# Kernel optimization log

Measured on AMD Instinct MI355X. Metric: run time of the kernel, lower is better.

The kernel has to match this reference:

```python
import jax, jax.numpy as jnp
import numpy as np

EPS = 1e-8

def squash(s, axis=-1):
    norm = jnp.linalg.norm(s, axis=axis, keepdims=True)
    scale = norm / (1.0 + norm * norm)
    return scale * s / (norm + EPS)

def setup_inputs() -> dict:
    key = jax.random.key(0)
    k1, k2, k3, k4 = jax.random.split(key, 4)
    B = 65536
    x = jax.random.normal(k1, (B, 210), dtype=jnp.float32)
    # stacked weights/biases for the 7 Linear(30,8) primary capsules
    W_pc = jax.random.normal(k2, (7, 8, 30), dtype=jnp.float32) * (1.0 / np.sqrt(30.0))
    b_pc = jax.random.normal(k3, (7, 8), dtype=jnp.float32) * 0.01
    W = jax.random.normal(k4, (7, 12, 8, 16), dtype=jnp.float32)
    return {"x": x, "W_pc": W_pc, "b_pc": b_pc, "W": W, "num_iterations": 3}

def reference(x, W_pc, b_pc, W, num_iterations):
    B = x.shape[0]
    groups = x.reshape(B, 7, 30)                              # [B,7,30]
    # 7 parallel Linear(30,8) + squash -> primary capsules u
    u = squash(jnp.einsum('bng,nog->bno', groups, W_pc) + b_pc)  # [B,7,8]
    # prediction vectors u_hat (expand over the 12 output capsules)
    u_hat = jnp.einsum('bnj,nmjk->bnmk', u, W)                # [B,7,12,16]
    b = jnp.zeros((B, 7, 12), dtype=x.dtype)
    v = None
    for it in range(num_iterations):
        c = jax.nn.softmax(b, axis=2)                         # [B,7,12]
        s = jnp.einsum('bnm,bnmk->bmk', c, u_hat)             # [B,12,16]
        v = squash(s)
        if it < num_iterations - 1:
            b = b + jnp.einsum('bnmk,bmk->bnm', u_hat, v)
    return jnp.linalg.norm(v, axis=-1)                        # [B,12]
```

## Files before the change

### kernel.cpp

```cpp
#include <hip/hip_runtime.h>
#include <math.h>

#define GPB 8
#define THREADS 256

template<int CTRL>
__device__ __forceinline__ float dpp_add(float x) {
    int xi = __builtin_bit_cast(int, x);
    int yi = __builtin_amdgcn_update_dpp(0, xi, CTRL, 0xF, 0xF, false);
    return x + __builtin_bit_cast(float, yi);
}
__device__ __forceinline__ float row16_sum(float x) {
    x = dpp_add<0x121>(x);
    x = dpp_add<0x122>(x);
    x = dpp_add<0x124>(x);
    x = dpp_add<0x128>(x);
    return x;
}
__device__ __forceinline__ float xor16_add(float x) {
    int y = __builtin_amdgcn_ds_swizzle(__builtin_bit_cast(int, x), 0x401F);
    return x + __builtin_bit_cast(float, y);
}
__device__ __forceinline__ float rcpf_(float x) { return __builtin_amdgcn_rcpf(x); }

__global__ void transpose_W_kernel(const float* __restrict__ W,
                                   float4* __restrict__ Wt) {
    int i = blockIdx.x * blockDim.x + threadIdx.x;
    if (i < 3584) {
        int l  = i & 31;
        int r  = i >> 5;
        int q  = r & 1;
        int j  = (r >> 1) & 7;
        int n  = r >> 4;
        int kh = l >> 4;
        int t  = l & 15;
        int mm = (t < 12) ? t : 11;
        const float* src = W + (((size_t)(n * 12 + mm) * 8 + j) * 16 + kh * 8 + q * 4);
        Wt[i] = *(const float4*)src;
    }
}

__global__ __launch_bounds__(THREADS) void capsnet_kernel(
    const float* __restrict__ x,
    const float* __restrict__ W_pc,
    const float* __restrict__ b_pc,
    const float4* __restrict__ Wt,
    const int*  __restrict__ p_niter,
    float* __restrict__ out,
    int B)
{
    __shared__ float xs[GPB][210];
    __shared__ float us[GPB][56];

    const int tid = threadIdx.x;
    const int g   = tid >> 5;
    const int l   = tid & 31;
    const int kh  = l >> 4;
    const int t   = l & 15;
    int b = blockIdx.x * GPB + g;
    const bool valid_b = (b < B);
    if (!valid_b) b = B - 1;
    const int niter = *p_niter;

    {
        const float2* xrow = (const float2*)(x + (size_t)b * 210);
        float2* xdst = (float2*)&xs[g][0];
        #pragma unroll
        for (int i = 0; i < 4; ++i) {
            int idx = l + 32 * i;
            if (idx < 105) xdst[idx] = xrow[idx];
        }
    }
    __syncthreads();

    #pragma unroll
    for (int i = 0; i < 2; ++i) {
        int idx = l + 32 * i;
        if (idx < 56) {
            int n = idx >> 3;
            const float2* wrow2 = (const float2*)(W_pc + idx * 30);
            const float2* xr2   = (const float2*)&xs[g][n * 30];
            float acc = b_pc[idx];
            #pragma unroll
            for (int gg = 0; gg < 15; ++gg) {
                float2 wv = wrow2[gg];
                float2 xv = xr2[gg];
                acc += xv.x * wv.x;
                acc += xv.y * wv.y;
            }
            us[g][idx] = acc;
        }
    }
    __syncthreads();

    if (l < 7) {
        float vals[8];
        float s2 = 0.f;
        #pragma unroll
        for (int o = 0; o < 8; ++o) {
            vals[o] = us[g][l * 8 + o];
            s2 += vals[o] * vals[o];
        }
        float nrm = sqrtf(s2);
        float f = nrm * rcpf_((1.f + s2) * (nrm + 1e-8f));
        #pragma unroll
        for (int o = 0; o < 8; ++o) us[g][l * 8 + o] = vals[o] * f;
    }
    __syncthreads();

    float uh[7][8];
    #pragma unroll
    for (int n = 0; n < 7; ++n) {
        float uu[8];
        {
            float4 a  = *(const float4*)&us[g][n * 8];
            float4 c4 = *(const float4*)&us[g][n * 8 + 4];
            uu[0] = a.x;  uu[1] = a.y;  uu[2] = a.z;  uu[3] = a.w;
            uu[4] = c4.x; uu[5] = c4.y; uu[6] = c4.z; uu[7] = c4.w;
        }
        #pragma unroll
        for (int kk = 0; kk < 8; ++kk) uh[n][kk] = 0.f;
        #pragma unroll
        for (int j = 0; j < 8; ++j) {
            float uj = uu[j];
            const float4* base = Wt + (size_t)(n * 8 + j) * 64 + l;
            float4 w0 = base[0];
            float4 w1 = base[32];
            uh[n][0] += uj * w0.x;  uh[n][1] += uj * w0.y;
            uh[n][2] += uj * w0.z;  uh[n][3] += uj * w0.w;
            uh[n][4] += uj * w1.x;  uh[n][5] += uj * w1.y;
            uh[n][6] += uj * w1.z;  uh[n][7] += uj * w1.w;
        }
    }

    const bool active = (t < 12);
    float blog[7];
    float vnorm = 0.f;

    {
        float s[8];
        #pragma unroll
        for (int kk = 0; kk < 8; ++kk) s[kk] = uh[0][kk];
        #pragma unroll
        for (int n = 1; n < 7; ++n)
            #pragma unroll
            for (int kk = 0; kk < 8; ++kk) s[kk] += uh[n][kk];
        const float c0 = 1.0f / 12.0f;
        #pragma unroll
        for (int kk = 0; kk < 8; ++kk) s[kk] *= c0;
        float s2l = 0.f;
        #pragma unroll
        for (int kk = 0; kk < 8; ++kk) s2l += s[kk] * s[kk];
        float s2 = xor16_add(s2l);
        float nrm = sqrtf(s2);
        float f = nrm * rcpf_((1.f + s2) * (nrm + 1e-8f));
        if (niter == 1) {
            vnorm = f * nrm;
        } else {
            #pragma unroll
            for (int kk = 0; kk < 8; ++kk) s[kk] *= f;
            #pragma unroll
            for (int n = 0; n < 7; ++n) {
                float dl = 0.f;
                #pragma unroll
                for (int kk = 0; kk < 8; ++kk) dl += uh[n][kk] * s[kk];
                blog[n] = xor16_add(dl);
            }
        }
    }

    for (int it = 1; it < niter; ++it) {
        float c[7];
        #pragma unroll
        for (int n = 0; n < 7; ++n) {
            float e  = active ? __expf(blog[n]) : 0.f;
            float sm = row16_sum(e);
            c[n] = e * rcpf_(sm);
        }
        float s[8];
        #pragma unroll
        for (int kk = 0; kk < 8; ++kk) s[kk] = 0.f;
        #pragma unroll
        for (int n = 0; n < 7; ++n) {
            float cn = c[n];
            #pragma unroll
            for (int kk = 0; kk < 8; ++kk) s[kk] += cn * uh[n][kk];
        }
        float s2l = 0.f;
        #pragma unroll
        for (int kk = 0; kk < 8; ++kk) s2l += s[kk] * s[kk];
        float s2 = xor16_add(s2l);
        float nrm = sqrtf(s2);
        float f = nrm * rcpf_((1.f + s2) * (nrm + 1e-8f));
        if (it == niter - 1) {
            vnorm = f * nrm;
        } else {
            #pragma unroll
            for (int kk = 0; kk < 8; ++kk) s[kk] *= f;
            #pragma unroll
            for (int n = 0; n < 7; ++n) {
                float dl = 0.f;
                #pragma unroll
                for (int kk = 0; kk < 8; ++kk) dl += uh[n][kk] * s[kk];
                blog[n] += xor16_add(dl);
            }
        }
    }

    if (active && (kh == 0) && valid_b) out[(size_t)b * 12 + t] = vnorm;
}

extern "C" void kernel_launch(void* const* d_in, const int* in_sizes, int n_in,
                              void* d_out, int out_size, void* d_ws, size_t ws_size,
                              hipStream_t stream) {
    const float* x    = (const float*)d_in[0];
    const float* W_pc = (const float*)d_in[1];
    const float* b_pc = (const float*)d_in[2];
    const float* W    = (const float*)d_in[3];
    const int* niter  = (const int*)d_in[4];
    float* out = (float*)d_out;

    float4* Wt = (float4*)d_ws;

    int B = in_sizes[0] / 210;
    int blocks = (B + GPB - 1) / GPB;

    transpose_W_kernel<<<14, 256, 0, stream>>>(W, Wt);
    capsnet_kernel<<<blocks, THREADS, 0, stream>>>(x, W_pc, b_pc, Wt, niter, out, B);
}
```

Before: 224.8 us.

## Process two batch elements per 32-lane group to reuse W loads

```diff
diff --git a/kernel.cpp b/kernel.cpp
--- a/kernel.cpp
+++ b/kernel.cpp
@@ -2,6 +2,7 @@
 #include <math.h>
 
 #define GPB 8
+#define EPG 2
 #define THREADS 256
 
 template<int CTRL>
@@ -49,165 +50,189 @@
     float* __restrict__ out,
     int B)
 {
-    __shared__ float xs[GPB][210];
-    __shared__ float us[GPB][56];
+    __shared__ float xs[GPB][420];
+    __shared__ float us[GPB][EPG][56];
 
     const int tid = threadIdx.x;
     const int g   = tid >> 5;
     const int l   = tid & 31;
     const int kh  = l >> 4;
     const int t   = l & 15;
-    int b = blockIdx.x * GPB + g;
-    const bool valid_b = (b < B);
-    if (!valid_b) b = B - 1;
+    int b0 = (blockIdx.x * GPB + g) * EPG;
+    if (b0 + 1 >= B) b0 = B - 2;
     const int niter = *p_niter;
 
     {
-        const float2* xrow = (const float2*)(x + (size_t)b * 210);
+        const float2* xrow = (const float2*)(x + (size_t)b0 * 210);
         float2* xdst = (float2*)&xs[g][0];
         #pragma unroll
-        for (int i = 0; i < 4; ++i) {
+        for (int i = 0; i < 7; ++i) {
             int idx = l + 32 * i;
-            if (idx < 105) xdst[idx] = xrow[idx];
+            if (idx < 210) xdst[idx] = xrow[idx];
         }
     }
     __syncthreads();
 
     #pragma unroll
-    for (int i = 0; i < 2; ++i) {
-        int idx = l + 32 * i;
-        if (idx < 56) {
-            int n = idx >> 3;
-            const float2* wrow2 = (const float2*)(W_pc + idx * 30);
-            const float2* xr2   = (const float2*)&xs[g][n * 30];
-            float acc = b_pc[idx];
-            #pragma unroll
-            for (int gg = 0; gg < 15; ++gg) {
-                float2 wv = wrow2[gg];
-                float2 xv = xr2[gg];
-                acc += xv.x * wv.x;
-                acc += xv.y * wv.y;
-            }
-            us[g][idx] = acc;
+    for (int e = 0; e < EPG; ++e) {
+        #pragma unroll
+        for (int i = 0; i < 2; ++i) {
+            int idx = l + 32 * i;
+            if (idx < 56) {
+                int n = idx >> 3;
+                const float2* wrow2 = (const float2*)(W_pc + idx * 30);
+                const float2* xr2   = (const float2*)&xs[g][e * 210 + n * 30];
+                float acc = b_pc[idx];
+                #pragma unroll
+                for (int gg = 0; gg < 15; ++gg) {
+                    float2 wv = wrow2[gg];
+                    float2 xv = xr2[gg];
+                    acc += xv.x * wv.x;
+                    acc += xv.y * wv.y;
+                }
+                us[g][e][idx] = acc;
+            }
         }
     }
     __syncthreads();
 
-    if (l < 7) {
-        float vals[8];
-        float s2 = 0.f;
-        #pragma unroll
-        for (int o = 0; o < 8; ++o) {
-            vals[o] = us[g][l * 8 + o];
-            s2 += vals[o] * vals[o];
-        }
-        float nrm = sqrtf(s2);
-        float f = nrm * rcpf_((1.f + s2) * (nrm + 1e-8f));
-        #pragma unroll
-        for (int o = 0; o < 8; ++o) us[g][l * 8 + o] = vals[o] * f;
+    {
+        int sn = l & 15;
+        int se = l >> 4;
+        if (sn < 7) {
+            float vals[8];
+            float s2 = 0.f;
+            #pragma unroll
+            for (int o = 0; o < 8; ++o) {
+                vals[o] = us[g][se][sn * 8 + o];
+                s2 += vals[o] * vals[o];
+            }
+            float nrm = sqrtf(s2);
+            float f = nrm * rcpf_((1.f + s2) * (nrm + 1e-8f));
+            #pragma unroll
+            for (int o = 0; o < 8; ++o) us[g][se][sn * 8 + o] = vals[o] * f;
+        }
     }
     __syncthreads();
 
-    float uh[7][8];
+    float uh[EPG][7][8];
     #pragma unroll
     for (int n = 0; n < 7; ++n) {
-        float uu[8];
-        {
-            float4 a  = *(const float4*)&us[g][n * 8];
-            float4 c4 = *(const float4*)&us[g][n * 8 + 4];
-            uu[0] = a.x;  uu[1] = a.y;  uu[2] = a.z;  uu[3] = a.w;
-            uu[4] = c4.x; uu[5] = c4.y; uu[6] = c4.z; uu[7] = c4.w;
-        }
-        #pragma unroll
-        for (int kk = 0; kk < 8; ++kk) uh[n][kk] = 0.f;
+        float uu[EPG][8];
+        #pragma unroll
+        for (int e = 0; e < EPG; ++e) {
+            float4 a  = *(const float4*)&us[g][e][n * 8];
+            float4 c4 = *(const float4*)&us[g][e][n * 8 + 4];
+            uu[e][0] = a.x;  uu[e][1] = a.y;  uu[e][2] = a.z;  uu[e][3] = a.w;
+            uu[e][4] = c4.x; uu[e][5] = c4.y; uu[e][6] = c4.z; uu[e][7] = c4.w;
+        }
+        #pragma unroll
+        for (int e = 0; e < EPG; ++e)
+            #pragma unroll
+            for (int kk = 0; kk < 8; ++kk) uh[e][n][kk] = 0.f;
         #pragma unroll
         for (int j = 0; j < 8; ++j) {
-            float uj = uu[j];
             const float4* base = Wt + (size_t)(n * 8 + j) * 64 + l;
             float4 w0 = base[0];
             float4 w1 = base[32];
-            uh[n][0] += uj * w0.x;  uh[n][1] += uj * w0.y;
-            uh[n][2] += uj * w0.z;  uh[n][3] += uj * w0.w;
-            uh[n][4] += uj * w1.x;  uh[n][5] += uj * w1.y;
-            uh[n][6] += uj * w1.z;  uh[n][7] += uj * w1.w;
+            #pragma unroll
+            for (int e = 0; e < EPG; ++e) {
+                float uj = uu[e][j];
+                uh[e][n][0] += uj * w0.x;  uh[e][n][1] += uj * w0.y;
+                uh[e][n][2] += uj * w0.z;  uh[e][n][3] += uj * w0.w;
+                uh[e][n][4] += uj * w1.x;  uh[e][n][5] += uj * w1.y;
+                uh[e][n][6] += uj * w1.z;  uh[e][n][7] += uj * w1.w;
+            }
         }
     }
 
     const bool active = (t < 12);
-    float blog[7];
-    float vnorm = 0.f;
+    float blog[EPG][7];
+    float vnorm[EPG];
+    #pragma unroll
+    for (int e = 0; e < EPG; ++e) vnorm[e] = 0.f;
 
     {
-        float s[8];
-        #pragma unroll
-        for (int kk = 0; kk < 8; ++kk) s[kk] = uh[0][kk];
-        #pragma unroll
-        for (int n = 1; n < 7; ++n)
-            #pragma unroll
-            for (int kk = 0; kk < 8; ++kk) s[kk] += uh[n][kk];
-        const float c0 = 1.0f / 12.0f;
-        #pragma unroll
-        for (int kk = 0; kk < 8; ++kk) s[kk] *= c0;
-        float s2l = 0.f;
-        #pragma unroll
-        for (int kk = 0; kk < 8; ++kk) s2l += s[kk] * s[kk];
-        float s2 = xor16_add(s2l);
-        float nrm = sqrtf(s2);
-        float f = nrm * rcpf_((1.f + s2) * (nrm + 1e-8f));
-        if (niter == 1) {
-            vnorm = f * nrm;
-        } else {
-            #pragma unroll
-            for (int kk = 0; kk < 8; ++kk) s[kk] *= f;
+        #pragma unroll
+        for (int e = 0; e < EPG; ++e) {
+            float s[8];
+            #pragma unroll
+            for (int kk = 0; kk < 8; ++kk) s[kk] = uh[e][0][kk];
+            #pragma unroll
+            for (int n = 1; n < 7; ++n)
+                #pragma unroll
+                for (int kk = 0; kk < 8; ++kk) s[kk] += uh[e][n][kk];
+            const float c0 = 1.0f / 12.0f;
+            #pragma unroll
+            for (int kk = 0; kk < 8; ++kk) s[kk] *= c0;
+            float s2l = 0.f;
+            #pragma unroll
+            for (int kk = 0; kk < 8; ++kk) s2l += s[kk] * s[kk];
+            float s2 = xor16_add(s2l);
+            float nrm = sqrtf(s2);
+            float f = nrm * rcpf_((1.f + s2) * (nrm + 1e-8f));
+            if (niter == 1) {
+                vnorm[e] = f * nrm;
+            } else {
+                #pragma unroll
+                for (int kk = 0; kk < 8; ++kk) s[kk] *= f;
+                #pragma unroll
+                for (int n = 0; n < 7; ++n) {
+                    float dl = 0.f;
+                    #pragma unroll
+                    for (int kk = 0; kk < 8; ++kk) dl += uh[e][n][kk] * s[kk];
+                    blog[e][n] = xor16_add(dl);
+                }
+            }
+        }
+    }
+
+    for (int it = 1; it < niter; ++it) {
+        #pragma unroll
+        for (int e = 0; e < EPG; ++e) {
+            float c[7];
             #pragma unroll
             for (int n = 0; n < 7; ++n) {
-                float dl = 0.f;
-                #pragma unroll
-                for (int kk = 0; kk < 8; ++kk) dl += uh[n][kk] * s[kk];
-                blog[n] = xor16_add(dl);
-            }
-        }
-    }
-
-    for (int it = 1; it < niter; ++it) {
-        float c[7];
-        #pragma unroll
-        for (int n = 0; n < 7; ++n) {
-            float e  = active ? __expf(blog[n]) : 0.f;
-            float sm = row16_sum(e);
-            c[n] = e * rcpf_(sm);
-        }
-        float s[8];
-        #pragma unroll
-        for (int kk = 0; kk < 8; ++kk) s[kk] = 0.f;
-        #pragma unroll
-        for (int n = 0; n < 7; ++n) {
-            float cn = c[n];
-            #pragma unroll
-            for (int kk = 0; kk < 8; ++kk) s[kk] += cn * uh[n][kk];
-        }
-        float s2l = 0.f;
-        #pragma unroll
-        for (int kk = 0; kk < 8; ++kk) s2l += s[kk] * s[kk];
-        float s2 = xor16_add(s2l);
-        float nrm = sqrtf(s2);
-        float f = nrm * rcpf_((1.f + s2) * (nrm + 1e-8f));
-        if (it == niter - 1) {
-            vnorm = f * nrm;
-        } else {
-            #pragma unroll
-            for (int kk = 0; kk < 8; ++kk) s[kk] *= f;
+                float ev = active ? __expf(blog[e][n]) : 0.f;
+                float sm = row16_sum(ev);
+                c[n] = ev * rcpf_(sm);
+            }
+            float s[8];
+            #pragma unroll
+            for (int kk = 0; kk < 8; ++kk) s[kk] = 0.f;
             #pragma unroll
             for (int n = 0; n < 7; ++n) {
-                float dl = 0.f;
-                #pragma unroll
-                for (int kk = 0; kk < 8; ++kk) dl += uh[n][kk] * s[kk];
-                blog[n] += xor16_add(dl);
-            }
-        }
-    }
-
-    if (active && (kh == 0) && valid_b) out[(size_t)b * 12 + t] = vnorm;
+                float cn = c[n];
+                #pragma unroll
+                for (int kk = 0; kk < 8; ++kk) s[kk] += cn * uh[e][n][kk];
+            }
+            float s2l = 0.f;
+            #pragma unroll
+            for (int kk = 0; kk < 8; ++kk) s2l += s[kk] * s[kk];
+            float s2 = xor16_add(s2l);
+            float nrm = sqrtf(s2);
+            float f = nrm * rcpf_((1.f + s2) * (nrm + 1e-8f));
+            if (it == niter - 1) {
+                vnorm[e] = f * nrm;
+            } else {
+                #pragma unroll
+                for (int kk = 0; kk < 8; ++kk) s[kk] *= f;
+                #pragma unroll
+                for (int n = 0; n < 7; ++n) {
+                    float dl = 0.f;
+                    #pragma unroll
+                    for (int kk = 0; kk < 8; ++kk) dl += uh[e][n][kk] * s[kk];
+                    blog[e][n] += xor16_add(dl);
+                }
+            }
+        }
+    }
+
+    if (active && (kh == 0)) {
+        #pragma unroll
+        for (int e = 0; e < EPG; ++e)
+            out[(size_t)(b0 + e) * 12 + t] = vnorm[e];
+    }
 }
 
 extern "C" void kernel_launch(void* const* d_in, const int* in_sizes, int n_in,
@@ -223,7 +248,8 @@
     float4* Wt = (float4*)d_ws;
 
     int B = in_sizes[0] / 210;
-    int blocks = (B + GPB - 1) / GPB;
+    int elems_per_block = GPB * EPG;
+    int blocks = (B + elems_per_block - 1) / elems_per_block;
 
     transpose_W_kernel<<<14, 256, 0, stream>>>(W, Wt);
     capsnet_kernel<<<blocks, THREADS, 0, stream>>>(x, W_pc, b_pc, Wt, niter, out, B);
```

After: 474.7 us. +111.2%, slower.

## Assign one full 64-lane wavefront per batch sample instead of half-wave

Applied to the files above, without the earlier changes.

```diff
diff --git a/kernel.cpp b/kernel.cpp
--- a/kernel.cpp
+++ b/kernel.cpp
@@ -1,7 +1,7 @@
 #include <hip/hip_runtime.h>
 #include <math.h>
 
-#define GPB 8
+#define WPB 4
 #define THREADS 256
 
 template<int CTRL>
@@ -17,9 +17,11 @@
     x = dpp_add<0x128>(x);
     return x;
 }
-__device__ __forceinline__ float xor16_add(float x) {
+__device__ __forceinline__ float kq_sum(float x) {
     int y = __builtin_amdgcn_ds_swizzle(__builtin_bit_cast(int, x), 0x401F);
-    return x + __builtin_bit_cast(float, y);
+    x += __builtin_bit_cast(float, y);
+    x += __shfl_xor(x, 32, 64);
+    return x;
 }
 __device__ __forceinline__ float rcpf_(float x) { return __builtin_amdgcn_rcpf(x); }
 
@@ -27,15 +29,14 @@
                                    float4* __restrict__ Wt) {
     int i = blockIdx.x * blockDim.x + threadIdx.x;
     if (i < 3584) {
-        int l  = i & 31;
-        int r  = i >> 5;
-        int q  = r & 1;
-        int j  = (r >> 1) & 7;
-        int n  = r >> 4;
-        int kh = l >> 4;
+        int l  = i & 63;
+        int r  = i >> 6;
+        int j  = r & 7;
+        int n  = r >> 3;
+        int kq = l >> 4;
         int t  = l & 15;
         int mm = (t < 12) ? t : 11;
-        const float* src = W + (((size_t)(n * 12 + mm) * 8 + j) * 16 + kh * 8 + q * 4);
+        const float* src = W + (((size_t)(n * 12 + mm) * 8 + j) * 16 + kq * 4);
         Wt[i] = *(const float4*)src;
     }
 }
@@ -49,47 +50,43 @@
     float* __restrict__ out,
     int B)
 {
-    __shared__ float xs[GPB][210];
-    __shared__ float us[GPB][56];
+    __shared__ float xs[WPB][210];
+    __shared__ float us[WPB][56];
 
     const int tid = threadIdx.x;
-    const int g   = tid >> 5;
-    const int l   = tid & 31;
-    const int kh  = l >> 4;
+    const int w   = tid >> 6;
+    const int l   = tid & 63;
+    const int kq  = l >> 4;
     const int t   = l & 15;
-    int b = blockIdx.x * GPB + g;
+    int b = blockIdx.x * WPB + w;
     const bool valid_b = (b < B);
     if (!valid_b) b = B - 1;
     const int niter = *p_niter;
 
     {
         const float2* xrow = (const float2*)(x + (size_t)b * 210);
-        float2* xdst = (float2*)&xs[g][0];
-        #pragma unroll
-        for (int i = 0; i < 4; ++i) {
-            int idx = l + 32 * i;
+        float2* xdst = (float2*)&xs[w][0];
+        #pragma unroll
+        for (int i = 0; i < 2; ++i) {
+            int idx = l + 64 * i;
             if (idx < 105) xdst[idx] = xrow[idx];
         }
     }
     __syncthreads();
 
-    #pragma unroll
-    for (int i = 0; i < 2; ++i) {
-        int idx = l + 32 * i;
-        if (idx < 56) {
-            int n = idx >> 3;
-            const float2* wrow2 = (const float2*)(W_pc + idx * 30);
-            const float2* xr2   = (const float2*)&xs[g][n * 30];
-            float acc = b_pc[idx];
-            #pragma unroll
-            for (int gg = 0; gg < 15; ++gg) {
-                float2 wv = wrow2[gg];
-                float2 xv = xr2[gg];
-                acc += xv.x * wv.x;
-                acc += xv.y * wv.y;
-            }
-            us[g][idx] = acc;
-        }
+    if (l < 56) {
+        int n = l >> 3;
+        const float2* wrow2 = (const float2*)(W_pc + l * 30);
+        const float2* xr2   = (const float2*)&xs[w][n * 30];
+        float acc = b_pc[l];
+        #pragma unroll
+        for (int gg = 0; gg < 15; ++gg) {
+            float2 wv = wrow2[gg];
+            float2 xv = xr2[gg];
+            acc += xv.x * wv.x;
+            acc += xv.y * wv.y;
+        }
+        us[w][l] = acc;
     }
     __syncthreads();
 
@@ -98,38 +95,34 @@
         float s2 = 0.f;
         #pragma unroll
         for (int o = 0; o < 8; ++o) {
-            vals[o] = us[g][l * 8 + o];
+            vals[o] = us[w][l * 8 + o];
             s2 += vals[o] * vals[o];
         }
         float nrm = sqrtf(s2);
         float f = nrm * rcpf_((1.f + s2) * (nrm + 1e-8f));
         #pragma unroll
-        for (int o = 0; o < 8; ++o) us[g][l * 8 + o] = vals[o] * f;
+        for (int o = 0; o < 8; ++o) us[w][l * 8 + o] = vals[o] * f;
     }
     __syncthreads();
 
-    float uh[7][8];
+    float uh[7][4];
     #pragma unroll
     for (int n = 0; n < 7; ++n) {
         float uu[8];
         {
-            float4 a  = *(const float4*)&us[g][n * 8];
-            float4 c4 = *(const float4*)&us[g][n * 8 + 4];
+            float4 a  = *(const float4*)&us[w][n * 8];
+            float4 c4 = *(const float4*)&us[w][n * 8 + 4];
             uu[0] = a.x;  uu[1] = a.y;  uu[2] = a.z;  uu[3] = a.w;
             uu[4] = c4.x; uu[5] = c4.y; uu[6] = c4.z; uu[7] = c4.w;
         }
         #pragma unroll
-        for (int kk = 0; kk < 8; ++kk) uh[n][kk] = 0.f;
+        for (int kk = 0; kk < 4; ++kk) uh[n][kk] = 0.f;
         #pragma unroll
         for (int j = 0; j < 8; ++j) {
+            float4 wv = Wt[(size_t)(n * 8 + j) * 64 + l];
             float uj = uu[j];
-            const float4* base = Wt + (size_t)(n * 8 + j) * 64 + l;
-            float4 w0 = base[0];
-            float4 w1 = base[32];
-            uh[n][0] += uj * w0.x;  uh[n][1] += uj * w0.y;
-            uh[n][2] += uj * w0.z;  uh[n][3] += uj * w0.w;
-            uh[n][4] += uj * w1.x;  uh[n][5] += uj * w1.y;
-            uh[n][6] += uj * w1.z;  uh[n][7] += uj * w1.w;
+            uh[n][0] += uj * wv.x;  uh[n][1] += uj * wv.y;
+            uh[n][2] += uj * wv.z;  uh[n][3] += uj * wv.w;
         }
     }
 
@@ -138,33 +131,33 @@
     float vnorm = 0.f;
 
     {
-        float s[8];
-        #pragma unroll
-        for (int kk = 0; kk < 8; ++kk) s[kk] = uh[0][kk];
+        float s[4];
+        #pragma unroll
+        for (int kk = 0; kk < 4; ++kk) s[kk] = uh[0][kk];
         #pragma unroll
         for (int n = 1; n < 7; ++n)
             #pragma unroll
-            for (int kk = 0; kk < 8; ++kk) s[kk] += uh[n][kk];
+            for (int kk = 0; kk < 4; ++kk) s[kk] += uh[n][kk];
         const float c0 = 1.0f / 12.0f;
         #pragma unroll
-        for (int kk = 0; kk < 8; ++kk) s[kk] *= c0;
+        for (int kk = 0; kk < 4; ++kk) s[kk] *= c0;
         float s2l = 0.f;
         #pragma unroll
-        for (int kk = 0; kk < 8; ++kk) s2l += s[kk] * s[kk];
-        float s2 = xor16_add(s2l);
+        for (int kk = 0; kk < 4; ++kk) s2l += s[kk] * s[kk];
+        float s2 = kq_sum(s2l);
         float nrm = sqrtf(s2);
         float f = nrm * rcpf_((1.f + s2) * (nrm + 1e-8f));
         if (niter == 1) {
             vnorm = f * nrm;
         } else {
             #pragma unroll
-            for (int kk = 0; kk < 8; ++kk) s[kk] *= f;
+            for (int kk = 0; kk < 4; ++kk) s[kk] *= f;
             #pragma unroll
             for (int n = 0; n < 7; ++n) {
                 float dl = 0.f;
                 #pragma unroll
-                for (int kk = 0; kk < 8; ++kk) dl += uh[n][kk] * s[kk];
-                blog[n] = xor16_add(dl);
+                for (int kk = 0; kk < 4; ++kk) dl += uh[n][kk] * s[kk];
+                blog[n] = kq_sum(dl);
             }
         }
     }
@@ -173,41 +166,41 @@
         float c[7];
         #pragma unroll
         for (int n = 0; n < 7; ++n) {
-            float e  = active ? __expf(blog[n]) : 0.f;
-            float sm = row16_sum(e);
-            c[n] = e * rcpf_(sm);
-        }
-        float s[8];
-        #pragma unroll
-        for (int kk = 0; kk < 8; ++kk) s[kk] = 0.f;
+            float ev = active ? __expf(blog[n]) : 0.f;
+            float sm = row16_sum(ev);
+            c[n] = ev * rcpf_(sm);
+        }
+        float s[4];
+        #pragma unroll
+        for (int kk = 0; kk < 4; ++kk) s[kk] = 0.f;
         #pragma unroll
         for (int n = 0; n < 7; ++n) {
             float cn = c[n];
             #pragma unroll
-            for (int kk = 0; kk < 8; ++kk) s[kk] += cn * uh[n][kk];
+            for (int kk = 0; kk < 4; ++kk) s[kk] += cn * uh[n][kk];
         }
         float s2l = 0.f;
         #pragma unroll
-        for (int kk = 0; kk < 8; ++kk) s2l += s[kk] * s[kk];
-        float s2 = xor16_add(s2l);
+        for (int kk = 0; kk < 4; ++kk) s2l += s[kk] * s[kk];
+        float s2 = kq_sum(s2l);
         float nrm = sqrtf(s2);
         float f = nrm * rcpf_((1.f + s2) * (nrm + 1e-8f));
         if (it == niter - 1) {
             vnorm = f * nrm;
         } else {
             #pragma unroll
-            for (int kk = 0; kk < 8; ++kk) s[kk] *= f;
+            for (int kk = 0; kk < 4; ++kk) s[kk] *= f;
             #pragma unroll
             for (int n = 0; n < 7; ++n) {
                 float dl = 0.f;
                 #pragma unroll
-                for (int kk = 0; kk < 8; ++kk) dl += uh[n][kk] * s[kk];
-                blog[n] += xor16_add(dl);
+                for (int kk = 0; kk < 4; ++kk) dl += uh[n][kk] * s[kk];
+                blog[n] += kq_sum(dl);
             }
         }
     }
 
-    if (active && (kh == 0) && valid_b) out[(size_t)b * 12 + t] = vnorm;
+    if (active && (kq == 0) && valid_b) out[(size_t)b * 12 + t] = vnorm;
 }
 
 extern "C" void kernel_launch(void* const* d_in, const int* in_sizes, int n_in,
@@ -223,7 +216,7 @@
     float4* Wt = (float4*)d_ws;
 
     int B = in_sizes[0] / 210;
-    int blocks = (B + GPB - 1) / GPB;
+    int blocks = (B + WPB - 1) / WPB;
 
     transpose_W_kernel<<<14, 256, 0, stream>>>(W, Wt);
     capsnet_kernel<<<blocks, THREADS, 0, stream>>>(x, W_pc, b_pc, Wt, niter, out, B);
```

Result: faster. 218.9 us (-2.6%).
